# Optimization experiments

Measured on AMD Instinct MI355X. Metric: run time of the kernel, lower is better.

The kernel has to match this reference:

```python
import jax, jax.numpy as jnp
import numpy as np

NFIELD = 40

def setup_inputs() -> dict:
    key = jax.random.key(0)
    ks = jax.random.split(key, 7)
    B, F, E, A = 1024, NFIELD, 128, 128
    s = 1.0 / np.sqrt(E)
    return {
        "x": jax.random.normal(ks[0], (B, F, E), dtype=jnp.float32),
        "attn_w_w": jax.random.normal(ks[1], (A, E), dtype=jnp.float32) * s,
        "attn_w_b": jax.random.normal(ks[2], (A,), dtype=jnp.float32) * s,
        "attn_h_w": jax.random.normal(ks[3], (1, A), dtype=jnp.float32) * s,
        "attn_h_b": jax.random.normal(ks[4], (1,), dtype=jnp.float32) * s,
        "attn_p_w": jax.random.normal(ks[5], (1, E), dtype=jnp.float32) * s,
        "attn_p_b": jax.random.normal(ks[6], (1,), dtype=jnp.float32) * s,
    }

def reference(x, attn_w_w, attn_w_b, attn_h_w, attn_h_b, attn_p_w, attn_p_b):
    # x: [B, F, E]; pairwise field interactions over upper-triangular (i<j) pairs
    nfield = x.shape[1]
    vi, vj = np.triu_indices(nfield, k=1)  # static index arrays, P = F*(F-1)/2
    hp = x[:, vi, :] * x[:, vj, :]                                   # [B, P, E]
    aw = jax.nn.relu(jnp.einsum('bpe,ae->bpa', hp, attn_w_w) + attn_w_b)  # [B, P, A]
    scores = jnp.einsum('bpa,oa->bpo', aw, attn_h_w) + attn_h_b          # [B, P, 1]
    attn = jax.nn.softmax(scores, axis=1)                                # softmax over pairs
    afm = jnp.sum(attn * hp, axis=1)                                     # [B, E]
    out = jnp.einsum('be,oe->bo', afm, attn_p_w) + attn_p_b              # [B, 1]
    return out.squeeze(1)                                                # [B]
```

## Files before the change

kernel.cpp:

```cpp
#include <hip/hip_runtime.h>
#include <hip/hip_fp16.h>

#define NF 40
#define NE 128
#define NA 128
#define NP 780
#define NPT 784
#define NMT 49
#define XS_LD 132
#define XS16_LD 136
#define G_LD 44

typedef _Float16 half8 __attribute__((ext_vector_type(8)));
typedef float floatx4 __attribute__((ext_vector_type(4)));

__device__ __forceinline__ float rowsum16(float x) {
    x += __int_as_float(__builtin_amdgcn_update_dpp(0, __float_as_int(x), 0x121, 0xf, 0xf, true));
    x += __int_as_float(__builtin_amdgcn_update_dpp(0, __float_as_int(x), 0x122, 0xf, 0xf, true));
    x += __int_as_float(__builtin_amdgcn_update_dpp(0, __float_as_int(x), 0x124, 0xf, 0xf, true));
    x += __int_as_float(__builtin_amdgcn_update_dpp(0, __float_as_int(x), 0x128, 0xf, 0xf, true));
    return x;
}

__global__ __launch_bounds__(256)
void afm_prep_kernel(const float* __restrict__ wg,
                     unsigned short* __restrict__ wbf,
                     int* __restrict__ ijg)
{
    const int t = blockIdx.x * 256 + threadIdx.x;
    if (t < NA * NE / 4) {
        float4 v = *(const float4*)(wg + t * 4);
        union { _Float16 h[4]; ushort4 u; } c;
        c.h[0] = (_Float16)v.x;
        c.h[1] = (_Float16)v.y;
        c.h[2] = (_Float16)v.z;
        c.h[3] = (_Float16)v.w;
        *(ushort4*)(wbf + t * 4) = c.u;
    }
    if (t < NPT) {
        int v = 0;
        if (t < NP) {
            int i = 0, rem = t;
            while (rem >= (NF - 1 - i)) { rem -= (NF - 1 - i); ++i; }
            v = (i << 8) | (i + 1 + rem);
        }
        ijg[t] = v;
    }
}

__global__ __launch_bounds__(256, 2)
void afm_fused_kernel(const float* __restrict__ xg,
                      const unsigned short* __restrict__ wbf,
                      const int* __restrict__ ijg,
                      const float* __restrict__ wbg,
                      const float* __restrict__ hg,
                      const float* __restrict__ pwg,
                      const float* __restrict__ pbg,
                      float* __restrict__ out)
{
    __shared__ float          xs[NF][XS_LD];
    __shared__ unsigned short xs16[NF][XS16_LD];
    __shared__ float sc[NPT];
    __shared__ int   ij[NPT];
    __shared__ float G[NF][G_LD];
    __shared__ float afmp[4][NE];
    __shared__ float red_max[4], red_sum[4], red_out[4];

    const int tid  = threadIdx.x;
    const int b    = blockIdx.x;
    const int lane = tid & 63;
    const int wid  = tid >> 6;
    const int col  = lane & 15;
    const int quad = (lane >> 4) & 3;

    const float* xb = xg + (size_t)b * (NF * NE);
    for (int t = tid; t < NF * (NE / 4); t += 256) {
        int row = t >> 5, c = (t & 31) * 4;
        float4 v = *(const float4*)(xb + row * NE + c);
        *(float4*)&xs[row][c] = v;
        union { _Float16 h[4]; unsigned long long ull; } cv;
        cv.h[0] = (_Float16)v.x;
        cv.h[1] = (_Float16)v.y;
        cv.h[2] = (_Float16)v.z;
        cv.h[3] = (_Float16)v.w;
        *(unsigned long long*)&xs16[row][c] = cv.ull;
    }
    if (tid < NPT / 4) {
        *(int4*)&ij[tid * 4] = ((const int4*)ijg)[tid];
    }
    float wbr[8], hr[8];
#pragma unroll
    for (int n = 0; n < 8; ++n) {
        wbr[n] = wbg[n * 16 + col];
        hr[n]  = hg[n * 16 + col];
    }
    half8 bfrag[8][4];
#pragma unroll
    for (int n = 0; n < 8; ++n)
#pragma unroll
        for (int k = 0; k < 4; ++k)
            bfrag[n][k] = *(const half8*)(const void*)(wbf + (n * 16 + col) * NE + k * 32 + quad * 8);
    __syncthreads();

    for (int mt = wid; mt < NMT; mt += 4) {
        const int p0 = mt * 16;
        const int v  = ij[p0 + col];
        const unsigned short* xi16 = &xs16[(v >> 8) & 255][0];
        const unsigned short* xj16 = &xs16[v & 255][0];

        floatx4 acc[8];
#pragma unroll
        for (int n = 0; n < 8; ++n)
            acc[n] = (floatx4){wbr[n], wbr[n], wbr[n], wbr[n]};

#pragma unroll
        for (int k = 0; k < 4; ++k) {
            const int koff = k * 32 + quad * 8;
            half8 ih = *(const half8*)(const void*)(xi16 + koff);
            half8 jh = *(const half8*)(const void*)(xj16 + koff);
            half8 af = ih * jh;
#pragma unroll
            for (int n = 0; n < 8; ++n)
                acc[n] = __builtin_amdgcn_mfma_f32_16x16x32_f16(af, bfrag[n][k], acc[n], 0, 0, 0);
        }

        float ps[4] = {0.f, 0.f, 0.f, 0.f};
#pragma unroll
        for (int n = 0; n < 8; ++n) {
#pragma unroll
            for (int r = 0; r < 4; ++r)
                ps[r] += fmaxf(acc[n][r], 0.f) * hr[n];
        }
#pragma unroll
        for (int r = 0; r < 4; ++r) ps[r] = rowsum16(ps[r]);
        if (col == 0) {
#pragma unroll
            for (int r = 0; r < 4; ++r) {
                int p = p0 + quad * 4 + r;
                if (p < NP) sc[p] = ps[r];
            }
        }
    }
    __syncthreads();

    float m = -1e30f;
    for (int p = tid; p < NP; p += 256) m = fmaxf(m, sc[p]);
#pragma unroll
    for (int off = 1; off < 64; off <<= 1) m = fmaxf(m, __shfl_xor(m, off));
    if (lane == 0) red_max[wid] = m;
    __syncthreads();
    const float M = fmaxf(fmaxf(red_max[0], red_max[1]), fmaxf(red_max[2], red_max[3]));

    float s = 0.f;
    for (int p = tid; p < NP; p += 256) {
        float e = __expf(sc[p] - M);
        sc[p] = e;
        s += e;
    }
#pragma unroll
    for (int off = 1; off < 64; off <<= 1) s += __shfl_xor(s, off);
    if (lane == 0) red_sum[wid] = s;
    __syncthreads();

    for (int p = tid; p < NP; p += 256) {
        int v = ij[p];
        float w = sc[p];
        G[(v >> 8) & 255][v & 255] = w;
        G[v & 255][(v >> 8) & 255] = w;
    }
    if (tid < NF) G[tid][tid] = 0.f;
    __syncthreads();

    {
        const int e2 = lane * 2;
        float2 xc[NF];
#pragma unroll
        for (int j = 0; j < NF; ++j) xc[j] = *(const float2*)&xs[j][e2];

        float a0 = 0.f, a1 = 0.f;
#pragma unroll
        for (int ii = 0; ii < 10; ++ii) {
            const int i = wid * 10 + ii;
            float y0 = 0.f, y1 = 0.f;
#pragma unroll
            for (int jj = 0; jj < 10; ++jj) {
                float4 g = *(const float4*)&G[i][jj * 4];
                y0 += g.x * xc[jj * 4 + 0].x;  y1 += g.x * xc[jj * 4 + 0].y;
                y0 += g.y * xc[jj * 4 + 1].x;  y1 += g.y * xc[jj * 4 + 1].y;
                y0 += g.z * xc[jj * 4 + 2].x;  y1 += g.z * xc[jj * 4 + 2].y;
                y0 += g.w * xc[jj * 4 + 3].x;  y1 += g.w * xc[jj * 4 + 3].y;
            }
            float2 xi = *(const float2*)&xs[i][e2];
            a0 += xi.x * y0;
            a1 += xi.y * y1;
        }
        *(float2*)&afmp[wid][e2] = make_float2(a0 * 0.5f, a1 * 0.5f);
    }
    __syncthreads();

    float vv = 0.f;
    if (tid < NE) {
        float a = afmp[0][tid] + afmp[1][tid] + afmp[2][tid] + afmp[3][tid];
        vv = a * pwg[tid];
    }
#pragma unroll
    for (int off = 1; off < 64; off <<= 1) vv += __shfl_xor(vv, off);
    if (lane == 0) red_out[wid] = vv;
    __syncthreads();
    if (tid == 0) {
        float S   = red_sum[0] + red_sum[1] + red_sum[2] + red_sum[3];
        float tot = red_out[0] + red_out[1] + red_out[2] + red_out[3];
        out[b] = tot / S + pbg[0];
    }
}

extern "C" void kernel_launch(void* const* d_in, const int* in_sizes, int n_in,
                              void* d_out, int out_size, void* d_ws, size_t ws_size,
                              hipStream_t stream) {
    const float* xg  = (const float*)d_in[0];
    const float* wg  = (const float*)d_in[1];
    const float* wbg = (const float*)d_in[2];
    const float* hg  = (const float*)d_in[3];
    const float* pwg = (const float*)d_in[5];
    const float* pbg = (const float*)d_in[6];
    const int B = in_sizes[0] / (NF * NE);

    unsigned short* wbf = (unsigned short*)d_ws;
    int* ijg = (int*)((char*)d_ws + NA * NE * sizeof(unsigned short));

    afm_prep_kernel<<<16, 256, 0, stream>>>(wg, wbf, ijg);
    afm_fused_kernel<<<B, 256, 0, stream>>>(xg, wbf, ijg, wbg, hg, pwg, pbg, (float*)d_out);
}
```

Baseline: 120.2 us.

## Split attention N-dim across wave pairs to cut registers and raise occupancy

Each wave now holds only half of the attention weight B-fragments (64 of 128 output columns) and iterates over every other M-tile. Partial scores go to two shared buffers that are summed during the max pass. The G scatter is folded into the exp pass, which removes one barrier, and the G·x loop is split into two j-halves to shrink the register footprint. Launch bounds go from 2 to 3 blocks per SU. The cost is extra shared memory, an extra pass over the summed partial scores, and each x pair product being recomputed by both halves.

```diff
diff --git a/kernel.cpp b/kernel.cpp
--- a/kernel.cpp
+++ b/kernel.cpp
@@ -48,7 +48,7 @@
     }
 }
 
-__global__ __launch_bounds__(256, 2)
+__global__ __launch_bounds__(256, 3)
 void afm_fused_kernel(const float* __restrict__ xg,
                       const unsigned short* __restrict__ wbf,
                       const int* __restrict__ ijg,
@@ -60,7 +60,8 @@
 {
     __shared__ float          xs[NF][XS_LD];
     __shared__ unsigned short xs16[NF][XS16_LD];
-    __shared__ float sc[NPT];
+    __shared__ float sc0[NPT];
+    __shared__ float sc1[NPT];
     __shared__ int   ij[NPT];
     __shared__ float G[NF][G_LD];
     __shared__ float afmp[4][NE];
@@ -72,6 +73,8 @@
     const int wid  = tid >> 6;
     const int col  = lane & 15;
     const int quad = (lane >> 4) & 3;
+    const int nhalf = wid >> 1;
+    const int wpar  = wid & 1;
 
     const float* xb = xg + (size_t)b * (NF * NE);
     for (int t = tid; t < NF * (NE / 4); t += 256) {
@@ -88,29 +91,31 @@
     if (tid < NPT / 4) {
         *(int4*)&ij[tid * 4] = ((const int4*)ijg)[tid];
     }
-    float wbr[8], hr[8];
-#pragma unroll
-    for (int n = 0; n < 8; ++n) {
-        wbr[n] = wbg[n * 16 + col];
-        hr[n]  = hg[n * 16 + col];
-    }
-    half8 bfrag[8][4];
-#pragma unroll
-    for (int n = 0; n < 8; ++n)
+    if (tid < NF) G[tid][tid] = 0.f;
+    float wbr[4], hr[4];
+#pragma unroll
+    for (int n = 0; n < 4; ++n) {
+        wbr[n] = wbg[nhalf * 64 + n * 16 + col];
+        hr[n]  = hg[nhalf * 64 + n * 16 + col];
+    }
+    half8 bfrag[4][4];
+#pragma unroll
+    for (int n = 0; n < 4; ++n)
 #pragma unroll
         for (int k = 0; k < 4; ++k)
-            bfrag[n][k] = *(const half8*)(const void*)(wbf + (n * 16 + col) * NE + k * 32 + quad * 8);
-    __syncthreads();
-
-    for (int mt = wid; mt < NMT; mt += 4) {
+            bfrag[n][k] = *(const half8*)(const void*)(wbf + (nhalf * 64 + n * 16 + col) * NE + k * 32 + quad * 8);
+    __syncthreads();
+
+    float* sch = nhalf ? sc1 : sc0;
+    for (int mt = wpar; mt < NMT; mt += 2) {
         const int p0 = mt * 16;
         const int v  = ij[p0 + col];
         const unsigned short* xi16 = &xs16[(v >> 8) & 255][0];
         const unsigned short* xj16 = &xs16[v & 255][0];
 
-        floatx4 acc[8];
-#pragma unroll
-        for (int n = 0; n < 8; ++n)
+        floatx4 acc[4];
+#pragma unroll
+        for (int n = 0; n < 4; ++n)
             acc[n] = (floatx4){wbr[n], wbr[n], wbr[n], wbr[n]};
 
 #pragma unroll
@@ -120,13 +125,13 @@
             half8 jh = *(const half8*)(const void*)(xj16 + koff);
             half8 af = ih * jh;
 #pragma unroll
-            for (int n = 0; n < 8; ++n)
+            for (int n = 0; n < 4; ++n)
                 acc[n] = __builtin_amdgcn_mfma_f32_16x16x32_f16(af, bfrag[n][k], acc[n], 0, 0, 0);
         }
 
         float ps[4] = {0.f, 0.f, 0.f, 0.f};
 #pragma unroll
-        for (int n = 0; n < 8; ++n) {
+        for (int n = 0; n < 4; ++n) {
 #pragma unroll
             for (int r = 0; r < 4; ++r)
                 ps[r] += fmaxf(acc[n][r], 0.f) * hr[n];
@@ -137,14 +142,18 @@
 #pragma unroll
             for (int r = 0; r < 4; ++r) {
                 int p = p0 + quad * 4 + r;
-                if (p < NP) sc[p] = ps[r];
+                if (p < NP) sch[p] = ps[r];
             }
         }
     }
     __syncthreads();
 
     float m = -1e30f;
-    for (int p = tid; p < NP; p += 256) m = fmaxf(m, sc[p]);
+    for (int p = tid; p < NP; p += 256) {
+        float full = sc0[p] + sc1[p];
+        sc0[p] = full;
+        m = fmaxf(m, full);
+    }
 #pragma unroll
     for (int off = 1; off < 64; off <<= 1) m = fmaxf(m, __shfl_xor(m, off));
     if (lane == 0) red_max[wid] = m;
@@ -153,8 +162,10 @@
 
     float s = 0.f;
     for (int p = tid; p < NP; p += 256) {
-        float e = __expf(sc[p] - M);
-        sc[p] = e;
+        int v = ij[p];
+        float e = __expf(sc0[p] - M);
+        G[(v >> 8) & 255][v & 255] = e;
+        G[v & 255][(v >> 8) & 255] = e;
         s += e;
     }
 #pragma unroll
@@ -162,37 +173,36 @@
     if (lane == 0) red_sum[wid] = s;
     __syncthreads();
 
-    for (int p = tid; p < NP; p += 256) {
-        int v = ij[p];
-        float w = sc[p];
-        G[(v >> 8) & 255][v & 255] = w;
-        G[v & 255][(v >> 8) & 255] = w;
-    }
-    if (tid < NF) G[tid][tid] = 0.f;
-    __syncthreads();
-
     {
         const int e2 = lane * 2;
-        float2 xc[NF];
-#pragma unroll
-        for (int j = 0; j < NF; ++j) xc[j] = *(const float2*)&xs[j][e2];
-
+        const int i0 = wid * 10;
+        float2 y[10];
+#pragma unroll
+        for (int r = 0; r < 10; ++r) y[r] = make_float2(0.f, 0.f);
+
+#pragma unroll
+        for (int jh2 = 0; jh2 < 2; ++jh2) {
+            float2 xc[20];
+#pragma unroll
+            for (int j = 0; j < 20; ++j) xc[j] = *(const float2*)&xs[jh2 * 20 + j][e2];
+#pragma unroll
+            for (int r = 0; r < 10; ++r) {
+#pragma unroll
+                for (int jj = 0; jj < 5; ++jj) {
+                    float4 g = *(const float4*)&G[i0 + r][jh2 * 20 + jj * 4];
+                    y[r].x += g.x * xc[jj * 4 + 0].x;  y[r].y += g.x * xc[jj * 4 + 0].y;
+                    y[r].x += g.y * xc[jj * 4 + 1].x;  y[r].y += g.y * xc[jj * 4 + 1].y;
+                    y[r].x += g.z * xc[jj * 4 + 2].x;  y[r].y += g.z * xc[jj * 4 + 2].y;
+                    y[r].x += g.w * xc[jj * 4 + 3].x;  y[r].y += g.w * xc[jj * 4 + 3].y;
+                }
+            }
+        }
         float a0 = 0.f, a1 = 0.f;
 #pragma unroll
-        for (int ii = 0; ii < 10; ++ii) {
-            const int i = wid * 10 + ii;
-            float y0 = 0.f, y1 = 0.f;
-#pragma unroll
-            for (int jj = 0; jj < 10; ++jj) {
-                float4 g = *(const float4*)&G[i][jj * 4];
-                y0 += g.x * xc[jj * 4 + 0].x;  y1 += g.x * xc[jj * 4 + 0].y;
-                y0 += g.y * xc[jj * 4 + 1].x;  y1 += g.y * xc[jj * 4 + 1].y;
-                y0 += g.z * xc[jj * 4 + 2].x;  y1 += g.z * xc[jj * 4 + 2].y;
-                y0 += g.w * xc[jj * 4 + 3].x;  y1 += g.w * xc[jj * 4 + 3].y;
-            }
-            float2 xi = *(const float2*)&xs[i][e2];
-            a0 += xi.x * y0;
-            a1 += xi.y * y1;
+        for (int r = 0; r < 10; ++r) {
+            float2 xi = *(const float2*)&xs[i0 + r][e2];
+            a0 += xi.x * y[r].x;
+            a1 += xi.y * y[r].y;
         }
         *(float2*)&afmp[wid][e2] = make_float2(a0 * 0.5f, a1 * 0.5f);
     }
```

Result: no change. 121.3 us (+0.9%).

## Compute pairwise attention sum via fp16 MFMA on symmetric weight matrix

Applied to the files above, without the earlier changes.

Replaces the scalar FP32 G·X product over the symmetric pair-weight matrix with fp16 MFMA tiles, storing the exponentiated softmax weights directly into a zero-padded fp16 G matrix. The max reduction is folded into the score loop, which removes the separate max pass over shared memory, and the G-fill pass merges into the exp pass, which removes a barrier. The exchange is reduced precision for the attention weights (fp16) and strided gathers from xs16 to build the B fragments.

```diff
diff --git a/kernel.cpp b/kernel.cpp
--- a/kernel.cpp
+++ b/kernel.cpp
@@ -9,7 +9,7 @@
 #define NMT 49
 #define XS_LD 132
 #define XS16_LD 136
-#define G_LD 44
+#define G16_LD 72
 
 typedef _Float16 half8 __attribute__((ext_vector_type(8)));
 typedef float floatx4 __attribute__((ext_vector_type(4)));
@@ -60,11 +60,11 @@
 {
     __shared__ float          xs[NF][XS_LD];
     __shared__ unsigned short xs16[NF][XS16_LD];
-    __shared__ float sc[NPT];
-    __shared__ int   ij[NPT];
-    __shared__ float G[NF][G_LD];
-    __shared__ float afmp[4][NE];
-    __shared__ float red_max[4], red_sum[4], red_out[4];
+    __shared__ float    sc[NPT];
+    __shared__ int      ij[NPT];
+    __shared__ _Float16 G16[48][G16_LD];
+    __shared__ float    afm1[NE];
+    __shared__ float red_max[4], red_sum[4], red_out[2];
 
     const int tid  = threadIdx.x;
     const int b    = blockIdx.x;
@@ -72,6 +72,9 @@
     const int wid  = tid >> 6;
     const int col  = lane & 15;
     const int quad = (lane >> 4) & 3;
+
+    for (int t = tid; t < 48 * G16_LD / 2; t += 256)
+        ((unsigned*)&G16[0][0])[t] = 0u;
 
     const float* xb = xg + (size_t)b * (NF * NE);
     for (int t = tid; t < NF * (NE / 4); t += 256) {
@@ -102,6 +105,7 @@
             bfrag[n][k] = *(const half8*)(const void*)(wbf + (n * 16 + col) * NE + k * 32 + quad * 8);
     __syncthreads();
 
+    float mloc = -1e30f;
     for (int mt = wid; mt < NMT; mt += 4) {
         const int p0 = mt * 16;
         const int v  = ij[p0 + col];
@@ -133,6 +137,13 @@
         }
 #pragma unroll
         for (int r = 0; r < 4; ++r) ps[r] = rowsum16(ps[r]);
+
+        float pm = -1e30f;
+#pragma unroll
+        for (int r = 0; r < 4; ++r)
+            pm = fmaxf(pm, (p0 + quad * 4 + r < NP) ? ps[r] : -1e30f);
+        mloc = fmaxf(mloc, pm);
+
         if (col == 0) {
 #pragma unroll
             for (int r = 0; r < 4; ++r) {
@@ -141,20 +152,19 @@
             }
         }
     }
-    __syncthreads();
-
-    float m = -1e30f;
-    for (int p = tid; p < NP; p += 256) m = fmaxf(m, sc[p]);
-#pragma unroll
-    for (int off = 1; off < 64; off <<= 1) m = fmaxf(m, __shfl_xor(m, off));
-    if (lane == 0) red_max[wid] = m;
+#pragma unroll
+    for (int off = 1; off < 64; off <<= 1) mloc = fmaxf(mloc, __shfl_xor(mloc, off));
+    if (lane == 0) red_max[wid] = mloc;
     __syncthreads();
     const float M = fmaxf(fmaxf(red_max[0], red_max[1]), fmaxf(red_max[2], red_max[3]));
 
     float s = 0.f;
     for (int p = tid; p < NP; p += 256) {
+        int v = ij[p];
         float e = __expf(sc[p] - M);
-        sc[p] = e;
+        _Float16 eh = (_Float16)e;
+        G16[(v >> 8) & 255][v & 255] = eh;
+        G16[v & 255][(v >> 8) & 255] = eh;
         s += e;
     }
 #pragma unroll
@@ -162,54 +172,59 @@
     if (lane == 0) red_sum[wid] = s;
     __syncthreads();
 
-    for (int p = tid; p < NP; p += 256) {
-        int v = ij[p];
-        float w = sc[p];
-        G[(v >> 8) & 255][v & 255] = w;
-        G[v & 255][(v >> 8) & 255] = w;
-    }
-    if (tid < NF) G[tid][tid] = 0.f;
-    __syncthreads();
-
     {
-        const int e2 = lane * 2;
-        float2 xc[NF];
-#pragma unroll
-        for (int j = 0; j < NF; ++j) xc[j] = *(const float2*)&xs[j][e2];
-
-        float a0 = 0.f, a1 = 0.f;
-#pragma unroll
-        for (int ii = 0; ii < 10; ++ii) {
-            const int i = wid * 10 + ii;
-            float y0 = 0.f, y1 = 0.f;
-#pragma unroll
-            for (int jj = 0; jj < 10; ++jj) {
-                float4 g = *(const float4*)&G[i][jj * 4];
-                y0 += g.x * xc[jj * 4 + 0].x;  y1 += g.x * xc[jj * 4 + 0].y;
-                y0 += g.y * xc[jj * 4 + 1].x;  y1 += g.y * xc[jj * 4 + 1].y;
-                y0 += g.z * xc[jj * 4 + 2].x;  y1 += g.z * xc[jj * 4 + 2].y;
-                y0 += g.w * xc[jj * 4 + 3].x;  y1 += g.w * xc[jj * 4 + 3].y;
+        const int n0 = wid * 2;
+        float af0 = 0.f, af1 = 0.f;
+#pragma unroll
+        for (int mt = 0; mt < 3; ++mt) {
+            const int arow = mt * 16 + col;
+            half8 a1 = *(const half8*)(const void*)&G16[arow][quad * 8];
+            half8 a2 = *(const half8*)(const void*)&G16[arow][32 + quad * 8];
+#pragma unroll
+            for (int nt = 0; nt < 2; ++nt) {
+                const int ecol = (n0 + nt) * 16 + col;
+                union { half8 h; unsigned short u[8]; } b1, b2;
+#pragma unroll
+                for (int j = 0; j < 8; ++j)
+                    b1.u[j] = xs16[quad * 8 + j][ecol];
+#pragma unroll
+                for (int j = 0; j < 8; ++j)
+                    b2.u[j] = 0;
+                if (quad == 0) {
+#pragma unroll
+                    for (int j = 0; j < 8; ++j)
+                        b2.u[j] = xs16[32 + j][ecol];
+                }
+                floatx4 y = (floatx4){0.f, 0.f, 0.f, 0.f};
+                y = __builtin_amdgcn_mfma_f32_16x16x32_f16(a1, b1.h, y, 0, 0, 0);
+                y = __builtin_amdgcn_mfma_f32_16x16x32_f16(a2, b2.h, y, 0, 0, 0);
+                if (mt * 16 + quad * 4 < NF) {
+                    float acc = 0.f;
+#pragma unroll
+                    for (int r = 0; r < 4; ++r)
+                        acc += xs[mt * 16 + quad * 4 + r][ecol] * y[r];
+                    if (nt == 0) af0 += acc; else af1 += acc;
+                }
             }
-            float2 xi = *(const float2*)&xs[i][e2];
-            a0 += xi.x * y0;
-            a1 += xi.y * y1;
-        }
-        *(float2*)&afmp[wid][e2] = make_float2(a0 * 0.5f, a1 * 0.5f);
+        }
+        af0 += __shfl_xor(af0, 16);  af0 += __shfl_xor(af0, 32);
+        af1 += __shfl_xor(af1, 16);  af1 += __shfl_xor(af1, 32);
+        if (lane < 16) {
+            afm1[(n0 + 0) * 16 + lane] = af0 * 0.5f;
+            afm1[(n0 + 1) * 16 + lane] = af1 * 0.5f;
+        }
     }
     __syncthreads();
 
     float vv = 0.f;
-    if (tid < NE) {
-        float a = afmp[0][tid] + afmp[1][tid] + afmp[2][tid] + afmp[3][tid];
-        vv = a * pwg[tid];
-    }
+    if (tid < NE) vv = afm1[tid] * pwg[tid];
 #pragma unroll
     for (int off = 1; off < 64; off <<= 1) vv += __shfl_xor(vv, off);
-    if (lane == 0) red_out[wid] = vv;
+    if (lane == 0 && wid < 2) red_out[wid] = vv;
     __syncthreads();
     if (tid == 0) {
         float S   = red_sum[0] + red_sum[1] + red_sum[2] + red_sum[3];
-        float tot = red_out[0] + red_out[1] + red_out[2] + red_out[3];
+        float tot = red_out[0] + red_out[1];
         out[b] = tot / S + pbg[0];
     }
 }
```

After: 116.3 us. -3.2%, faster.
